# Optimization experiments

Measured on AMD Instinct MI355X. Metric: run time of the kernel, lower is better.

The kernel has to match this reference:

```python
import jax, jax.numpy as jnp
import numpy as np
import math

F, H, N_CURR = 16384, 64, 8192
BOUNDARY = -0.01


def setup_inputs() -> dict:
    key = jax.random.key(0)
    ks = jax.random.split(key, 12)
    he_w = math.sqrt(2.0 / (H + 1))
    he_t = math.sqrt(2.0)
    return {
        "X": jax.random.normal(ks[0], (F,), jnp.float32),
        "delta": jax.random.uniform(ks[1], (F,), jnp.float32),
        "Ht": jax.random.normal(ks[2], (F, H), jnp.float32),
        "c_t": jax.random.normal(ks[3], (H,), jnp.float32),
        "c_global": jax.random.normal(ks[4], (F, H), jnp.float32),
        "lstm_weights": he_w * jax.random.normal(ks[5], (F, 3 * H, H + 1), jnp.float32),
        "lstm_bias": jnp.zeros((F, 3 * H), jnp.float32),
        "lstm_xT_weights": he_t * jax.random.normal(ks[6], (F, 2 * H, 1), jnp.float32),
        "lstm_xT_bias": jnp.zeros((F, 2 * H), jnp.float32),
        "lstm_delT_weights": he_t * jax.random.normal(ks[7], (F, 3 * H, 1), jnp.float32),
        "lstm_c_inp_weights": jax.random.normal(ks[8], (F, H), jnp.float32),
        "lstm_c_out_weights": jax.random.normal(ks[9], (F, H), jnp.float32),
        "feat_idx": jnp.arange(N_CURR, dtype=jnp.int32),
    }


def reference(X, delta, Ht, c_t, c_global, lstm_weights, lstm_bias,
              lstm_xT_weights, lstm_xT_bias, lstm_delT_weights,
              lstm_c_inp_weights, lstm_c_out_weights, feat_idx):
    # weight constraint on the hidden_size-th row of delT weights (clip to <= boundary)
    delT_w = lstm_delT_weights.at[:, H, :].set(
        jnp.minimum(lstm_delT_weights[:, H, :], BOUNDARY))

    x = X[feat_idx]                                   # [n]
    h_prev = Ht[feat_idx]                             # [n, H]
    cur_input = jnp.concatenate([x[:, None], h_prev], axis=-1)   # [n, H+1]

    # gathered per-feature small matvecs
    cur_out = jnp.einsum('ngh,nh->ng', lstm_weights[feat_idx], cur_input) \
        + lstm_bias[feat_idx]                          # [n, 3H]
    xm_out = lstm_xT_weights[feat_idx, :, 0] * x[:, None] + lstm_xT_bias[feat_idx]   # [n, 2H]
    dT_out = delT_w[feat_idx, :, 0] * delta[feat_idx][:, None]                        # [n, 3H]

    gate_input, gate_output, gate_pre_c = jnp.split(cur_out, 3, axis=-1)
    xm_T1, xm_T2 = jnp.split(xm_out, 2, axis=-1)
    del_T1, del_T2, del_To = jnp.split(dT_out, 3, axis=-1)

    T_1t = jax.nn.sigmoid(xm_T1 + jax.nn.sigmoid(del_T1))
    T_2t = jax.nn.sigmoid(xm_T2 + jax.nn.sigmoid(del_T2))
    gate_input = jax.nn.sigmoid(gate_input + lstm_c_inp_weights[feat_idx] * c_t)
    gate_pre_c = jnp.tanh(gate_pre_c)

    c_tilde = (1.0 - gate_input * T_1t) * c_t + gate_input * T_1t * gate_pre_c
    c_new = (1.0 - gate_input) * c_t + gate_input * T_2t * gate_pre_c
    gate_output = jax.nn.sigmoid(
        gate_output + lstm_c_out_weights[feat_idx] * c_tilde + del_To)

    h_new = gate_output * jnp.tanh(c_tilde)            # [n, H]

    H_curr = jnp.zeros_like(Ht).at[feat_idx].set(h_new)     # scatter into [F, H]
    c_global_new = c_global.at[feat_idx].set(c_new)
    C_curr = jnp.mean(c_new, axis=0)                   # aggregate_by='Mean' -> [H]
    return H_curr, c_global_new, C_curr
```

## Files before the change

kernel.cpp:

```cpp
#include <hip/hip_runtime.h>
#include <cstdint>
#include <cstddef>

#define HH 64
#define G2 128
#define G3 192
#define WROW 65
#define ROWF 12480
#define BOUNDARY (-0.01f)

__device__ __forceinline__ float sigm(float x) { return 1.0f / (1.0f + __expf(-x)); }

__global__ __launch_bounds__(256) void init_kernel(float* __restrict__ outH,
                                                   float* __restrict__ outC,
                                                   const float* __restrict__ c_global,
                                                   int fh4) {
    int idx = blockIdx.x * 256 + threadIdx.x;
    int stride = gridDim.x * 256;
    for (int k = idx; k < fh4; k += stride) {
        ((float4*)outH)[k] = make_float4(0.f, 0.f, 0.f, 0.f);
        ((float4*)outC)[k] = ((const float4*)c_global)[k];
    }
}

__global__ __launch_bounds__(256) void lstm_main(
    const float* __restrict__ X, const float* __restrict__ delta,
    const float* __restrict__ Ht, const float* __restrict__ c_t,
    const float* __restrict__ W, const float* __restrict__ bias,
    const float* __restrict__ xTw, const float* __restrict__ xTb,
    const float* __restrict__ dTw, const float* __restrict__ cinw,
    const float* __restrict__ coutw, const int* __restrict__ feat_idx,
    float* __restrict__ outH, float* __restrict__ outC) {

    __shared__ __align__(16) float inp[68];
    __shared__ float co[G3];

    const int t = threadIdx.x;
    const int i = feat_idx[blockIdx.x];
    const size_t i1 = (size_t)i * HH;
    const size_t i2 = (size_t)i * G2;
    const size_t i3 = (size_t)i * G3;

    float xi = 0.f, di = 0.f, ct = 0.f, cinv = 0.f, coutv = 0.f;
    float xw1 = 0.f, xw2 = 0.f, xb1 = 0.f, xb2 = 0.f;
    float dw1 = 0.f, dw2 = 0.f, dwo = 0.f, b0 = 0.f, b1 = 0.f, b2 = 0.f;
    if (t < HH) {
        xi = X[i];  di = delta[i];  ct = c_t[t];
        cinv = cinw[i1 + t];  coutv = coutw[i1 + t];
        xw1 = xTw[i2 + t];  xw2 = xTw[i2 + HH + t];
        xb1 = xTb[i2 + t];  xb2 = xTb[i2 + HH + t];
        dw1 = dTw[i3 + t];  dw2 = dTw[i3 + HH + t];  dwo = dTw[i3 + 2 * HH + t];
        b0 = bias[i3 + t];  b1 = bias[i3 + HH + t];  b2 = bias[i3 + 2 * HH + t];
    }

    if (t == 0) inp[0] = X[i];
    if (t >= 64 && t < 128) inp[1 + (t - 64)] = Ht[i1 + (t - 64)];
    __syncthreads();

    {
        const int G = t >> 4, j = t & 15;
        const float in0 = inp[j], in1 = inp[j + 16], in2 = inp[j + 32], in3 = inp[j + 48];
        const float in4 = inp[64];
        const float* wp = W + (size_t)i * ROWF + G * WROW + j;
        #pragma unroll 4
        for (int k = 0; k < 12; ++k) {
            const float* wr = wp + k * (16 * WROW);
            float acc = wr[0] * in0;
            acc = fmaf(wr[16], in1, acc);
            acc = fmaf(wr[32], in2, acc);
            acc = fmaf(wr[48], in3, acc);
            if (j == 0) acc = fmaf(wr[64 - j], in4, acc);
            acc += __shfl_xor(acc, 1);
            acc += __shfl_xor(acc, 2);
            acc += __shfl_xor(acc, 4);
            acc += __shfl_xor(acc, 8);
            if (j == 0) co[G + 16 * k] = acc;
        }
    }
    __syncthreads();

    if (t < HH) {
        float gi_pre = co[t] + b0;
        float go_pre = co[HH + t] + b1;
        float gc     = tanhf(co[2 * HH + t] + b2);

        float xm1 = fmaf(xw1, xi, xb1);
        float xm2 = fmaf(xw2, xi, xb2);
        if (t == 0) dw2 = fminf(dw2, BOUNDARY);

        float T1 = sigm(xm1 + sigm(dw1 * di));
        float T2 = sigm(xm2 + sigm(dw2 * di));
        float gi = sigm(gi_pre + cinv * ct);

        float gT1     = gi * T1;
        float c_tilde = (1.f - gT1) * ct + gT1 * gc;
        float c_new   = (1.f - gi) * ct + gi * T2 * gc;
        float go      = sigm(go_pre + coutv * c_tilde + dwo * di);

        outH[i1 + t] = go * tanhf(c_tilde);
        outC[i1 + t] = c_new;
    }
}

__global__ __launch_bounds__(256) void reduceA(const float* __restrict__ outC,
                                               const int* __restrict__ feat_idx,
                                               float* __restrict__ partial, int n) {
    __shared__ float s[256];
    const int b = blockIdx.x, t = threadIdx.x;
    const int h = t & 63, g = t >> 6;
    const int rend = min(n, (b + 1) * 64);
    float acc = 0.f;
    for (int r = b * 64 + g; r < rend; r += 4)
        acc += outC[(size_t)feat_idx[r] * HH + h];
    s[t] = acc;
    __syncthreads();
    if (t < HH) partial[b * HH + h] = s[h] + s[64 + h] + s[128 + h] + s[192 + h];
}

__global__ __launch_bounds__(256) void reduceB(const float* __restrict__ partial,
                                               float* __restrict__ outM,
                                               int nblocks, int n) {
    __shared__ float s[256];
    const int t = threadIdx.x, h = t & 63, g = t >> 6;
    float acc = 0.f;
    for (int b = g; b < nblocks; b += 4) acc += partial[(size_t)b * HH + h];
    s[t] = acc;
    __syncthreads();
    if (t < HH) outM[h] = (s[h] + s[64 + h] + s[128 + h] + s[192 + h]) / (float)n;
}

__global__ __launch_bounds__(256) void reduceAll(const float* __restrict__ outC,
                                                 const int* __restrict__ feat_idx,
                                                 float* __restrict__ outM, int n) {
    __shared__ float s[256];
    const int t = threadIdx.x, h = t & 63, g = t >> 6;
    float acc = 0.f;
    for (int r = g; r < n; r += 4)
        acc += outC[(size_t)feat_idx[r] * HH + h];
    s[t] = acc;
    __syncthreads();
    if (t < HH) outM[h] = (s[h] + s[64 + h] + s[128 + h] + s[192 + h]) / (float)n;
}

extern "C" void kernel_launch(void* const* d_in, const int* in_sizes, int n_in,
                              void* d_out, int out_size, void* d_ws, size_t ws_size,
                              hipStream_t stream) {
    const float* X        = (const float*)d_in[0];
    const float* delta    = (const float*)d_in[1];
    const float* Ht       = (const float*)d_in[2];
    const float* c_t      = (const float*)d_in[3];
    const float* c_global = (const float*)d_in[4];
    const float* W        = (const float*)d_in[5];
    const float* bias     = (const float*)d_in[6];
    const float* xTw      = (const float*)d_in[7];
    const float* xTb      = (const float*)d_in[8];
    const float* dTw      = (const float*)d_in[9];
    const float* cinw     = (const float*)d_in[10];
    const float* coutw    = (const float*)d_in[11];
    const int*   feat_idx = (const int*)d_in[12];

    const int F  = in_sizes[0];
    const int n  = in_sizes[12];
    const int FH = F * HH;

    float* out  = (float*)d_out;
    float* outH = out;
    float* outC = out + FH;
    float* outM = out + 2 * FH;

    {
        int fh4 = FH / 4;
        int blocks = (fh4 + 255) / 256;
        if (blocks > 2048) blocks = 2048;
        init_kernel<<<blocks, 256, 0, stream>>>(outH, outC, c_global, fh4);
    }

    lstm_main<<<n, 256, 0, stream>>>(X, delta, Ht, c_t, W, bias, xTw, xTb,
                                     dTw, cinw, coutw, feat_idx, outH, outC);

    int nA = (n + 63) / 64;
    if (ws_size >= (size_t)nA * HH * sizeof(float)) {
        float* partial = (float*)d_ws;
        reduceA<<<nA, 256, 0, stream>>>(outC, feat_idx, partial, n);
        reduceB<<<1, 256, 0, stream>>>(partial, outM, nA, n);
    } else {
        reduceAll<<<1, 256, 0, stream>>>(outC, feat_idx, outM, n);
    }
}
```

Measured before the change: 117.7 us.

## Use persistent blocks with register-prefetched weight tiles staged through LDS

```diff
diff --git a/kernel.cpp b/kernel.cpp
--- a/kernel.cpp
+++ b/kernel.cpp
@@ -5,11 +5,58 @@
 #define HH 64
 #define G2 128
 #define G3 192
-#define WROW 65
 #define ROWF 12480
+#define ROW4 3120
+#define CH4 520
+#define WZF 6240
 #define BOUNDARY (-0.01f)
+#define NBLK 1536
 
 __device__ __forceinline__ float sigm(float x) { return 1.0f / (1.0f + __expf(-x)); }
+
+struct Ops {
+    float xv, di, ct, cin, cou, xw1, xw2, xb1, xb2, dw1, dw2, dwo, bb;
+};
+
+#define WADDR(g) (b4 + (size_t)(((g) >= 2*CH4) ? 2*CH4 : (((g) >= CH4) ? CH4 : 0)) + (g))
+
+#define LOAD_OPS(o, ff, hhalf)                                            \
+    do {                                                                  \
+        const int h_ = ((hhalf) << 5) + (w << 4) + j;                     \
+        if (gt) {                                                         \
+            const size_t i1_ = (size_t)(ff) * HH;                         \
+            const size_t i2_ = (size_t)(ff) * G2;                         \
+            const size_t i3_ = (size_t)(ff) * G3;                         \
+            o.xv = X[ff]; o.di = delta[ff]; o.ct = c_t[h_];               \
+            o.cin = cinw[i1_ + h_]; o.cou = coutw[i1_ + h_];              \
+            o.xw1 = xTw[i2_ + h_]; o.xw2 = xTw[i2_ + HH + h_];            \
+            o.xb1 = xTb[i2_ + h_]; o.xb2 = xTb[i2_ + HH + h_];            \
+            o.dw1 = dTw[i3_ + h_]; o.dw2 = dTw[i3_ + HH + h_];            \
+            o.dwo = dTw[i3_ + 2 * HH + h_];                               \
+        }                                                                 \
+        if (mv) o.bb = bias[(size_t)(ff) * G3 + (c << 6) + h_];           \
+    } while (0)
+
+#define LOAD_W(ff, hhalf)                                                 \
+    do {                                                                  \
+        const size_t b4 = (size_t)(ff) * ROW4 + (size_t)(hhalf) * CH4;    \
+        r0 = W4[WADDR(t)];                                                \
+        r1 = W4[WADDR(256 + t)];                                          \
+        r2 = W4[WADDR(512 + t)];                                          \
+        r3 = W4[WADDR(768 + t)];                                          \
+        r4 = W4[WADDR(1024 + t)];                                         \
+        r5 = W4[WADDR(1280 + t)];                                         \
+        if (t < 24) r6 = W4[WADDR(1536 + t)];                             \
+    } while (0)
+
+#define WRITE_W_INP()                                                     \
+    do {                                                                  \
+        wz4[t] = r0; wz4[256 + t] = r1; wz4[512 + t] = r2;                \
+        wz4[768 + t] = r3; wz4[1024 + t] = r4; wz4[1280 + t] = r5;        \
+        if (t < 24) wz4[1536 + t] = r6;                                   \
+        if (t < HH) inp[1 + t] = nhv;                                     \
+        if (t == 0) inp[0] = nxx;                                         \
+    } while (0)
 
 __global__ __launch_bounds__(256) void init_kernel(float* __restrict__ outH,
                                                    float* __restrict__ outC,
@@ -23,82 +70,99 @@
     }
 }
 
-__global__ __launch_bounds__(256) void lstm_main(
+__global__ __launch_bounds__(256, 4) void lstm_persist(
     const float* __restrict__ X, const float* __restrict__ delta,
     const float* __restrict__ Ht, const float* __restrict__ c_t,
     const float* __restrict__ W, const float* __restrict__ bias,
     const float* __restrict__ xTw, const float* __restrict__ xTb,
     const float* __restrict__ dTw, const float* __restrict__ cinw,
     const float* __restrict__ coutw, const int* __restrict__ feat_idx,
-    float* __restrict__ outH, float* __restrict__ outC) {
-
-    __shared__ __align__(16) float inp[68];
-    __shared__ float co[G3];
+    float* __restrict__ outH, float* __restrict__ outC, int NI)
+{
+    __shared__ __align__(16) float wz[WZF];
+    __shared__ float inp[HH + 4];
 
     const int t = threadIdx.x;
-    const int i = feat_idx[blockIdx.x];
-    const size_t i1 = (size_t)i * HH;
-    const size_t i2 = (size_t)i * G2;
-    const size_t i3 = (size_t)i * G3;
-
-    float xi = 0.f, di = 0.f, ct = 0.f, cinv = 0.f, coutv = 0.f;
-    float xw1 = 0.f, xw2 = 0.f, xb1 = 0.f, xb2 = 0.f;
-    float dw1 = 0.f, dw2 = 0.f, dwo = 0.f, b0 = 0.f, b1 = 0.f, b2 = 0.f;
-    if (t < HH) {
-        xi = X[i];  di = delta[i];  ct = c_t[t];
-        cinv = cinw[i1 + t];  coutv = coutw[i1 + t];
-        xw1 = xTw[i2 + t];  xw2 = xTw[i2 + HH + t];
-        xb1 = xTb[i2 + t];  xb2 = xTb[i2 + HH + t];
-        dw1 = dTw[i3 + t];  dw2 = dTw[i3 + HH + t];  dwo = dTw[i3 + 2 * HH + t];
-        b0 = bias[i3 + t];  b1 = bias[i3 + HH + t];  b2 = bias[i3 + 2 * HH + t];
-    }
-
-    if (t == 0) inp[0] = X[i];
-    if (t >= 64 && t < 128) inp[1 + (t - 64)] = Ht[i1 + (t - 64)];
-    __syncthreads();
+    const int w = t >> 6;
+    const int l = t & 63;
+    const int c = l >> 4;
+    const int j = l & 15;
+    const bool mv = (w < 2) && (c < 3);
+    const bool gt = (w < 2) && (c == 0);
+
+    int item = blockIdx.x;
+    if (item >= NI) return;
+
+    const float4* W4 = (const float4*)W;
+    float4* wz4 = (float4*)wz;
+
+    float4 r0, r1, r2, r3, r4, r5;
+    float4 r6 = make_float4(0.f, 0.f, 0.f, 0.f);
+    Ops nx = {}, cu = {};
+    float nhv = 0.f, nxx = 0.f;
 
     {
-        const int G = t >> 4, j = t & 15;
-        const float in0 = inp[j], in1 = inp[j + 16], in2 = inp[j + 32], in3 = inp[j + 48];
-        const float in4 = inp[64];
-        const float* wp = W + (size_t)i * ROWF + G * WROW + j;
-        #pragma unroll 4
-        for (int k = 0; k < 12; ++k) {
-            const float* wr = wp + k * (16 * WROW);
-            float acc = wr[0] * in0;
-            acc = fmaf(wr[16], in1, acc);
-            acc = fmaf(wr[32], in2, acc);
-            acc = fmaf(wr[48], in3, acc);
-            if (j == 0) acc = fmaf(wr[64 - j], in4, acc);
-            acc += __shfl_xor(acc, 1);
-            acc += __shfl_xor(acc, 2);
-            acc += __shfl_xor(acc, 4);
-            acc += __shfl_xor(acc, 8);
-            if (j == 0) co[G + 16 * k] = acc;
+        const int f = feat_idx[item >> 1];
+        const int half = item & 1;
+        LOAD_W(f, half);
+        LOAD_OPS(nx, f, half);
+        if (t < HH) nhv = Ht[(size_t)f * HH + t];
+        if (t == 0) nxx = X[f];
+    }
+    WRITE_W_INP();
+    cu = nx;
+    __syncthreads();
+
+    for (;;) {
+        const int next = item + NBLK;
+        const bool more = (next < NI);
+        if (more) {
+            const int f = feat_idx[next >> 1];
+            const int half = next & 1;
+            LOAD_W(f, half);
+            LOAD_OPS(nx, f, half);
+            if (t < HH) nhv = Ht[(size_t)f * HH + t];
+            if (t == 0) nxx = X[f];
         }
-    }
-    __syncthreads();
-
-    if (t < HH) {
-        float gi_pre = co[t] + b0;
-        float go_pre = co[HH + t] + b1;
-        float gc     = tanhf(co[2 * HH + t] + b2);
-
-        float xm1 = fmaf(xw1, xi, xb1);
-        float xm2 = fmaf(xw2, xi, xb2);
-        if (t == 0) dw2 = fminf(dw2, BOUNDARY);
-
-        float T1 = sigm(xm1 + sigm(dw1 * di));
-        float T2 = sigm(xm2 + sigm(dw2 * di));
-        float gi = sigm(gi_pre + cinv * ct);
-
-        float gT1     = gi * T1;
-        float c_tilde = (1.f - gT1) * ct + gT1 * gc;
-        float c_new   = (1.f - gi) * ct + gi * T2 * gc;
-        float go      = sigm(go_pre + coutv * c_tilde + dwo * di);
-
-        outH[i1 + t] = go * tanhf(c_tilde);
-        outC[i1 + t] = c_new;
+        __builtin_amdgcn_sched_barrier(0);
+
+        {
+            const int f = feat_idx[item >> 1];
+            const int half = item & 1;
+            float acc = cu.bb;
+            if (mv) {
+                const float* wr = &wz[c * 2080 + ((w << 4) + j) * 65];
+                #pragma unroll
+                for (int e = 0; e < 65; ++e) acc = fmaf(wr[e], inp[e], acc);
+            }
+            if (w < 2) {
+                const float go_pre = __shfl(acc, 16 + j);
+                const float gc_pre = __shfl(acc, 32 + j);
+                if (gt) {
+                    const int h = (half << 5) + (w << 4) + j;
+                    const size_t i1 = (size_t)f * HH;
+                    float gc  = tanhf(gc_pre);
+                    float xm1 = fmaf(cu.xw1, cu.xv, cu.xb1);
+                    float xm2 = fmaf(cu.xw2, cu.xv, cu.xb2);
+                    float dw2 = (h == 0) ? fminf(cu.dw2, BOUNDARY) : cu.dw2;
+                    float T1 = sigm(xm1 + sigm(cu.dw1 * cu.di));
+                    float T2 = sigm(xm2 + sigm(dw2 * cu.di));
+                    float gi = sigm(acc + cu.cin * cu.ct);
+                    float gT1     = gi * T1;
+                    float c_tilde = (1.f - gT1) * cu.ct + gT1 * gc;
+                    float c_new   = (1.f - gi) * cu.ct + gi * T2 * gc;
+                    float go      = sigm(go_pre + cu.cou * c_tilde + cu.dwo * cu.di);
+                    outH[i1 + h] = go * tanhf(c_tilde);
+                    outC[i1 + h] = c_new;
+                }
+            }
+        }
+        if (!more) break;
+        __syncthreads();
+        WRITE_W_INP();
+        cu = nx;
+        __syncthreads();
+        item = next;
     }
 }
 
@@ -162,6 +226,7 @@
     const int F  = in_sizes[0];
     const int n  = in_sizes[12];
     const int FH = F * HH;
+    const int NI = 2 * n;
 
     float* out  = (float*)d_out;
     float* outH = out;
@@ -175,8 +240,12 @@
         init_kernel<<<blocks, 256, 0, stream>>>(outH, outC, c_global, fh4);
     }
 
-    lstm_main<<<n, 256, 0, stream>>>(X, delta, Ht, c_t, W, bias, xTw, xTb,
-                                     dTw, cinw, coutw, feat_idx, outH, outC);
+    {
+        int blocks = (NI < NBLK) ? NI : NBLK;
+        lstm_persist<<<blocks, 256, 0, stream>>>(X, delta, Ht, c_t, W, bias,
+                                                 xTw, xTb, dTw, cinw, coutw,
+                                                 feat_idx, outH, outC, NI);
+    }
 
     int nA = (n + 63) / 64;
     if (ws_size >= (size_t)nA * HH * sizeof(float)) {
```

After: 114.9 us. 2.4% less time.
